# Performance work log

Measured on AMD Instinct MI355X. Metric: run time of the kernel, lower is better.

The kernel has to match this reference:

```python
import jax, jax.numpy as jnp
import numpy as np

B, NC, F, U = 8, 64, 8, 128   # batch, mesh size, ConvLSTM filters, LSTM units
NITER = 4
BS = 200.0                    # box size
B1, B2, LR, EPS = 0.9, 0.999, 0.1, 1e-7


def _conv3d(x, w, b=None):
    out = jax.lax.conv_general_dilated(x, w, (1, 1, 1), 'SAME',
                                       dimension_numbers=('NDHWC', 'DHWIO', 'NDHWC'))
    return out if b is None else out + b


def _conv1d(x, w, b):
    return jax.lax.conv_general_dilated(x, w, (1,), 'SAME',
                                        dimension_numbers=('NWC', 'WIO', 'NWC')) + b


def setup_inputs():
    key = jax.random.key(0)
    ks = jax.random.split(key, 16)
    # radial |k| bin map, values in [0, NC)
    kf = np.fft.fftfreq(NC) * NC
    kx, ky, kz = np.meshgrid(kf, kf, kf, indexing='ij')
    knorm = np.sqrt(kx ** 2 + ky ** 2 + kz ** 2)
    kbinmap = np.minimum((knorm / knorm.max() * (NC - 1)).astype(np.int32), NC - 1)
    s = 0.05
    return {
        'x_init': jax.random.normal(ks[0], (B, NC, NC, NC), jnp.float32),
        'y':      jax.random.normal(ks[1], (B, NC, NC, NC), jnp.float32),
        'x_true': jax.random.normal(ks[2], (B, NC, NC, NC), jnp.float32),
        'kbinmap': jnp.asarray(kbinmap),
        # input_layer: Conv3D 2 -> F
        'W_in': jax.random.normal(ks[3], (3, 3, 3, 2, F), jnp.float32) * s,
        'b_in': jnp.zeros((F,), jnp.float32),
        # ConvLSTM3D cell: gates order i,f,g,o
        'Wx3': jax.random.normal(ks[4], (3, 3, 3, F, 4 * F), jnp.float32) * s,
        'Wh3': jax.random.normal(ks[5], (3, 3, 3, F, 4 * F), jnp.float32) * s,
        'b3':  jnp.zeros((4 * F,), jnp.float32),
        # output_layer: Conv3D F -> 1
        'W_out': jax.random.normal(ks[6], (3, 3, 3, F, 1), jnp.float32) * s,
        'b_out': jnp.zeros((1,), jnp.float32),
        # input_layer1d: Dense 2*NC -> U
        'Wd1': jax.random.normal(ks[7], (2 * NC, U), jnp.float32) * s,
        'bd1': jnp.zeros((U,), jnp.float32),
        # LSTM cell (units U)
        'Wlx': jax.random.normal(ks[8], (U, 4 * U), jnp.float32) * s,
        'Wlh': jax.random.normal(ks[9], (U, 4 * U), jnp.float32) * s,
        'bl':  jnp.zeros((4 * U,), jnp.float32),
        # output_layer1d: Dense U -> NC
        'Wd2': jax.random.normal(ks[10], (U, NC), jnp.float32) * s,
        'bd2': jnp.zeros((NC,), jnp.float32),
        # output_layer1dconv: Conv1D 1 -> 1, kernel 3
        'Wc1': jax.random.normal(ks[11], (3, 1, 1), jnp.float32) * s,
        'bc1': jnp.zeros((1,), jnp.float32),
    }


def _forward(x_init, y, x_true, W_in, b_in, Wx3, Wh3, b3, W_out, b_out,
             Wd1, bd1, Wlx, Wlh, bl, Wd2, bd2, Wc1, bc1, kbinmap):
    nc = x_init.shape[-1]
    bsz = x_init.shape[0]
    kflat = kbinmap.reshape(-1)
    counts = jax.ops.segment_sum(jnp.ones(kflat.shape, jnp.float32), kflat,
                                 num_segments=nc)

    def varmap(x):
        # tfvarmap: binned power spectrum, [B, nc]
        pm = jnp.abs(jnp.fft.fftn(x, axes=(1, 2, 3)) / nc ** 3) ** 2
        pmf = pm.reshape(bsz, -1)
        power = jax.vmap(lambda p: jax.ops.segment_sum(p, kflat, num_segments=nc))(pmf)
        return power / counts

    def filt(x, ps, p):
        # colorps (p=+0.5) / whitenps (p=-0.5); flowpm r2c/c2r norms cancel
        pmesh = ps[:, kbinmap]                      # [B,nc,nc,nc] gather by kbin
        fac = (pmesh ** p).astype(jnp.complex64)
        return jnp.real(jnp.fft.ifftn(jnp.fft.fftn(x, axes=(1, 2, 3)) * fac,
                                      axes=(1, 2, 3)))

    def convlstm(x, h, c):
        z = _conv3d(x, Wx3, b3) + _conv3d(h, Wh3)
        i, f, g, o = jnp.split(z, 4, axis=-1)
        c = jax.nn.sigmoid(f) * c + jax.nn.sigmoid(i) * jnp.tanh(g)
        h = jax.nn.sigmoid(o) * jnp.tanh(c)
        return h, c

    def lstm(x, h, c):
        z = x @ Wlx + h @ Wlh + bl
        i, f, g, o = jnp.split(z, 4, axis=-1)
        c = jax.nn.sigmoid(f) * c + jax.nn.sigmoid(i) * jnp.tanh(g)
        h = jax.nn.sigmoid(o) * jnp.tanh(c)
        return h, c

    ln10 = jnp.log(jnp.float32(10.0))

    def step(carry, t):
        pos, m, v, h1, c1, h3, c3, loss = carry
        grad = pos - y                              # stand-in grad_fn (data-consistency)
        m = B1 * m + (1.0 - B1) * grad
        v = B2 * v + (1.0 - B2) * grad * grad
        mc = m / (1.0 - B1 ** t)
        vc = v / (1.0 - B2 ** t)
        delta = -LR * mc / (jnp.sqrt(vc) + EPS)
        pspos = varmap(pos)
        psdelta = varmap(delta)
        lpspos = jnp.log(pspos * BS ** 3) / ln10
        lpsdelta = jnp.log(psdelta * BS ** 3) / ln10
        # 3D branch
        cell_in = _conv3d(jnp.stack([pos, delta], axis=-1), W_in, b_in)
        h3, c3 = convlstm(cell_in, h3, c3)
        delta_poswhite = _conv3d(h3, W_out, b_out)[..., 0]
        # 1D power-spectrum branch
        x1 = jnp.concatenate([lpspos, lpsdelta], axis=-1) @ Wd1 + bd1
        h1, c1 = lstm(x1, h1, c1)
        lps = h1 @ Wd2 + bd2
        lps = _conv1d(lps[..., None], Wc1, bc1)[..., 0]
        psdeltanew = jnp.exp(lps)                   # note: exp (base e), as in source
        new_pos = pos + filt(delta_poswhite, psdeltanew, 0.5)
        loss = loss + jnp.mean((x_true - new_pos) ** 2)
        return (new_pos, m, v, h1, c1, h3, c3, loss), None

    z = jnp.zeros_like(x_init)
    init = (x_init, z, z,
            jnp.zeros((bsz, U), x_init.dtype), jnp.zeros((bsz, U), x_init.dtype),
            jnp.zeros(x_init.shape + (F,), x_init.dtype),
            jnp.zeros(x_init.shape + (F,), x_init.dtype),
            jnp.zeros((), x_init.dtype))
    ts = jnp.arange(1, NITER + 1, dtype=jnp.float32)
    (pos, m, v, h1, c1, h3, c3, loss), _ = jax.lax.scan(step, init, ts)
    return pos, loss


def reference(x_init, y, x_true, kbinmap, W_in, b_in, Wx3, Wh3, b3, W_out, b_out,
              Wd1, bd1, Wlx, Wlh, bl, Wd2, bd2, Wc1, bc1):
    return _forward(x_init, y, x_true, W_in, b_in, Wx3, Wh3, b3, W_out, b_out,
                    Wd1, bd1, Wlx, Wlh, bl, Wd2, bd2, Wc1, bc1, kbinmap)
```

## Files before the change

### kernel.cpp

```cpp
#include <hip/hip_runtime.h>
#include <math.h>

#define NCC 64
#define NB 8
#define VOL (NCC*NCC*NCC)
#define TOT (NB*VOL)
#define WTOT 170869
#define PI2 6.2831853071795864769f
#define HS 287496
#define SX 4356

typedef unsigned short u16;
typedef __bf16 bf16x8 __attribute__((ext_vector_type(8)));
typedef float f32x16 __attribute__((ext_vector_type(16)));

__device__ __forceinline__ float b2f(u16 h){ return __uint_as_float(((unsigned)h)<<16); }
__device__ __forceinline__ u16 f2b(float f){
  unsigned u = __float_as_uint(f);
  unsigned r = (u + 0x7FFFu + ((u>>16)&1u)) >> 16;
  return (u16)r;
}
__device__ __forceinline__ float fsig(float x){ return 1.f / (1.f + __expf(-x)); }
__device__ __forceinline__ float ftanh(float x){
  float e = __expf(2.f * x);
  return 1.f - 2.f / (e + 1.f);
}

template<bool INV>
__device__ __forceinline__ void fft8(float2* x) {
  const float C = 0.70710678118654752440f;
  float2 s0,s1,s2,s3,s4,s5,s6,s7;
  s0 = make_float2(x[0].x + x[4].x, x[0].y + x[4].y);
  s4 = make_float2(x[0].x - x[4].x, x[0].y - x[4].y);
  s1 = make_float2(x[1].x + x[5].x, x[1].y + x[5].y);
  s5 = make_float2(x[1].x - x[5].x, x[1].y - x[5].y);
  s2 = make_float2(x[2].x + x[6].x, x[2].y + x[6].y);
  s6 = make_float2(x[2].x - x[6].x, x[2].y - x[6].y);
  s3 = make_float2(x[3].x + x[7].x, x[3].y + x[7].y);
  s7 = make_float2(x[3].x - x[7].x, x[3].y - x[7].y);
  float2 n5, n6, n7;
  if (!INV) {
    n5 = make_float2(C*(s5.x + s5.y), C*(s5.y - s5.x));
    n6 = make_float2(s6.y, -s6.x);
    n7 = make_float2(C*(s7.y - s7.x), -C*(s7.x + s7.y));
  } else {
    n5 = make_float2(C*(s5.x - s5.y), C*(s5.y + s5.x));
    n6 = make_float2(-s6.y, s6.x);
    n7 = make_float2(-C*(s7.x + s7.y), C*(s7.x - s7.y));
  }
  float2 t0,t1,t2,t3,t4,t5,t6,t7,d;
  t0 = make_float2(s0.x + s2.x, s0.y + s2.y);
  t2 = make_float2(s0.x - s2.x, s0.y - s2.y);
  t1 = make_float2(s1.x + s3.x, s1.y + s3.y);
  d  = make_float2(s1.x - s3.x, s1.y - s3.y);
  t3 = INV ? make_float2(-d.y, d.x) : make_float2(d.y, -d.x);
  t4 = make_float2(s4.x + n6.x, s4.y + n6.y);
  t6 = make_float2(s4.x - n6.x, s4.y - n6.y);
  t5 = make_float2(n5.x + n7.x, n5.y + n7.y);
  d  = make_float2(n5.x - n7.x, n5.y - n7.y);
  t7 = INV ? make_float2(-d.y, d.x) : make_float2(d.y, -d.x);
  x[0] = make_float2(t0.x + t1.x, t0.y + t1.y);
  x[1] = make_float2(t0.x - t1.x, t0.y - t1.y);
  x[2] = make_float2(t2.x + t3.x, t2.y + t3.y);
  x[3] = make_float2(t2.x - t3.x, t2.y - t3.y);
  x[4] = make_float2(t4.x + t5.x, t4.y + t5.y);
  x[5] = make_float2(t4.x - t5.x, t4.y - t5.y);
  x[6] = make_float2(t6.x + t7.x, t6.y + t7.y);
  x[7] = make_float2(t6.x - t7.x, t6.y - t7.y);
}

template<bool INV>
__device__ __forceinline__ void dft64(float2* Pf, const float2* tw, int ls, int ns) {
  const int BR[8] = {0,4,2,6,1,5,3,7};
  int t = threadIdx.x;
  int L0 = t >> 3, b = t & 7, L1 = L0 + 32;
  float2 v0[8], v1[8];
  #pragma unroll
  for (int a = 0; a < 8; ++a) v0[a] = Pf[L0*ls + (8*a + b)*ns];
  #pragma unroll
  for (int a = 0; a < 8; ++a) v1[a] = Pf[L1*ls + (8*a + b)*ns];
  __syncthreads();
  fft8<INV>(v0); fft8<INV>(v1);
  #pragma unroll
  for (int r = 0; r < 8; ++r) {
    float2 w = tw[(b * r) & 63];
    if (INV) w.y = -w.y;
    float2 a0 = v0[BR[r]], a1 = v1[BR[r]];
    Pf[L0*ls + (8*b + r)*ns] = make_float2(a0.x*w.x - a0.y*w.y, a0.x*w.y + a0.y*w.x);
    Pf[L1*ls + (8*b + r)*ns] = make_float2(a1.x*w.x - a1.y*w.y, a1.x*w.y + a1.y*w.x);
  }
  __syncthreads();
  int r = t & 7;
  #pragma unroll
  for (int q = 0; q < 8; ++q) v0[q] = Pf[L0*ls + (8*q + r)*ns];
  #pragma unroll
  for (int q = 0; q < 8; ++q) v1[q] = Pf[L1*ls + (8*q + r)*ns];
  fft8<INV>(v0); fft8<INV>(v1);
  #pragma unroll
  for (int j = 0; j < 8; ++j) {
    Pf[L0*ls + (8*BR[j] + r)*ns] = v0[j];
    Pf[L1*ls + (8*BR[j] + r)*ns] = v1[j];
  }
  __syncthreads();
}

__global__ __launch_bounds__(256) void k_sniff(const u16* __restrict__ x, int* __restrict__ flag) {
  __shared__ int cnt;
  if (threadIdx.x == 0) cnt = 0;
  __syncthreads();
  int sane = 0;
  for (int i = threadIdx.x; i < 1024; i += 256) {
    u16 h = x[2 * i];
    int e = (h >> 7) & 0xFF;
    if (h == 0 || (e >= 0x68 && e <= 0x8F)) sane++;
  }
  atomicAdd(&cnt, sane);
  __syncthreads();
  if (threadIdx.x == 0) flag[0] = (cnt >= 768) ? 1 : 0;
}

__global__ __launch_bounds__(256) void k_cvt(const void* __restrict__ in, size_t eoff,
                                             float* __restrict__ out, const int* __restrict__ flag) {
  size_t i = (size_t)blockIdx.x * 256 + threadIdx.x;
  if (*flag) out[i] = b2f(((const u16*)in)[eoff + i]);
  else       out[i] = ((const float*)in)[eoff + i];
}

__global__ __launch_bounds__(256) void k_cvtall(
    const void* s0, const void* s1, const void* s2, const void* s3,
    const void* s4, const void* s5, const void* s6, const void* s7,
    const void* s8, const void* s9, const void* s10, const void* s11,
    const void* s12, const void* s13, const void* s14, const void* s15,
    float* __restrict__ out, const int* __restrict__ flag) {
  const void* ps[16] = {s0,s1,s2,s3,s4,s5,s6,s7,s8,s9,s10,s11,s12,s13,s14,s15};
  const int offs[17] = {0,432,440,7352,14264,14296,14512,14513,30897,31025,
                        96561,162097,162609,170801,170865,170868,170869};
  int i = blockIdx.x * 256 + threadIdx.x;
  if (i >= WTOT) return;
  int s = 0;
  #pragma unroll
  for (int k = 1; k < 16; ++k) if (i >= offs[k]) s = k;
  int j = i - offs[s];
  if (*flag) out[i] = b2f(((const u16*)ps[s])[j]);
  else       out[i] = ((const float*)ps[s])[j];
}

__global__ __launch_bounds__(256) void k_mkwf(const void* __restrict__ Wx, const void* __restrict__ Wh,
                                              const int* __restrict__ flag, u16* __restrict__ Wf) {
  int i = blockIdx.x * 256 + threadIdx.x;
  if (i >= 13824) return;
  int j = i & 7, co = (i >> 3) & 31, hi = (i >> 8) & 1, tap = i >> 9;
  int src = tap * 256 + j * 32 + co;
  const void* P = hi ? Wh : Wx;
  u16 val;
  if (*flag) val = ((const u16*)P)[src];
  else       val = f2b(((const float*)P)[src]);
  Wf[i] = val;
}

__global__ __launch_bounds__(256) void k_mkwfo(const void* __restrict__ Wo,
                                               const int* __restrict__ flag, u16* __restrict__ Wfo) {
  int i = blockIdx.x * 256 + threadIdx.x;
  if (i >= 7168) return;
  int j = i & 7, co = (i >> 3) & 31, hi = (i >> 8) & 1, p = i >> 9;
  int tap = 2 * p + hi;
  u16 val = 0;
  if (co == 0 && tap < 27) {
    int src = tap * 8 + j;
    val = *flag ? ((const u16*)Wo)[src] : f2b(((const float*)Wo)[src]);
  }
  Wfo[i] = val;
}

__global__ __launch_bounds__(256) void k_mkwfi(const void* __restrict__ Wi,
                                               const int* __restrict__ flag, u16* __restrict__ Wfi) {
  int i = blockIdx.x * 256 + threadIdx.x;
  if (i >= 2048) return;
  int j = i & 7, co = (i >> 3) & 31, hi = (i >> 8) & 1, m = i >> 9;
  int k = hi * 8 + j;
  int tap = m * 8 + (k >> 1), ch = k & 1;
  u16 val = 0;
  if (co < 8 && tap < 27) {
    int src = tap * 16 + ch * 8 + co;
    val = *flag ? ((const u16*)Wi)[src] : f2b(((const float*)Wi)[src]);
  }
  Wfi[i] = val;
}

__global__ __launch_bounds__(256) void k_counts(const int* __restrict__ kbin,
                                                float* __restrict__ cnts) {
  __shared__ float s[NCC];
  int t = threadIdx.x;
  if (t < NCC) s[t] = 0.f;
  __syncthreads();
  int i = blockIdx.x * 256 + t;
  atomicAdd(&s[kbin[i]], 1.f);
  __syncthreads();
  if (t < NCC) atomicAdd(&cnts[t], s[t]);
}

__global__ __launch_bounds__(256) void k_fft_zy_adam(
    const float* __restrict__ pos, const void* __restrict__ yraw, size_t yoff,
    float* __restrict__ m, float* __restrict__ v, float* __restrict__ dpw,
    float2* __restrict__ cout, float ib1, float ib2, int first,
    const int* __restrict__ flag, float* __restrict__ psp, float* __restrict__ psd) {
  __shared__ float2 P[64*66];
  __shared__ float2 tw[64];
  int t = threadIdx.x;
  if (t < 64) { float s, c; __sincosf(-(PI2/64.f)*(float)t, &s, &c); tw[t] = make_float2(c, s); }
  int bb = blockIdx.x >> 6, xx = blockIdx.x & 63;
  if (xx == 0) {
    if (t < 64)                 psp[bb*64 + t] = 0.f;
    else if (t < 128)           psd[bb*64 + (t - 64)] = 0.f;
  }
  size_t pb = (size_t)blockIdx.x * 4096;
  int bf = *flag;
  #pragma unroll
  for (int i = 0; i < 4; ++i) {
    int i4 = t + 256*i;
    float4 p4 = ((const float4*)(pos + pb))[i4];
    float yv[4];
    if (bf) {
      uint2 yu = ((const uint2*)((const u16*)yraw + yoff + pb))[i4];
      const u16* yp = (const u16*)&yu;
      yv[0]=b2f(yp[0]); yv[1]=b2f(yp[1]); yv[2]=b2f(yp[2]); yv[3]=b2f(yp[3]);
    } else {
      float4 y4 = ((const float4*)((const float*)yraw + yoff + pb))[i4];
      yv[0]=y4.x; yv[1]=y4.y; yv[2]=y4.z; yv[3]=y4.w;
    }
    float pv[4] = {p4.x, p4.y, p4.z, p4.w};
    float mo[4], vo[4], dd[4];
    if (!first) {
      float4 m4 = ((const float4*)(m + pb))[i4];
      float4 v4 = ((const float4*)(v + pb))[i4];
      mo[0]=m4.x; mo[1]=m4.y; mo[2]=m4.z; mo[3]=m4.w;
      vo[0]=v4.x; vo[1]=v4.y; vo[2]=v4.z; vo[3]=v4.w;
    }
    #pragma unroll
    for (int c = 0; c < 4; ++c) {
      float g = pv[c] - yv[c];
      float mi = first ? 0.1f*g : 0.9f*mo[c] + 0.1f*g;
      float vi = first ? 0.001f*g*g : 0.999f*vo[c] + 0.001f*g*g;
      mo[c] = mi; vo[c] = vi;
      dd[c] = -0.1f * (mi * ib1) / (sqrtf(vi * ib2) + 1e-7f);
    }
    ((float4*)(m + pb))[i4]   = make_float4(mo[0], mo[1], mo[2], mo[3]);
    ((float4*)(v + pb))[i4]   = make_float4(vo[0], vo[1], vo[2], vo[3]);
    ((float4*)(dpw + pb))[i4] = make_float4(dd[0], dd[1], dd[2], dd[3]);
    int base = i4 * 4;
    float2* row = P + (base >> 6)*66 + (base & 63);
    row[0] = make_float2(pv[0], 0.f);
    row[1] = make_float2(pv[1], 0.f);
    row[2] = make_float2(pv[2], 0.f);
    row[3] = make_float2(pv[3], 0.f);
  }
  __syncthreads();
  dft64<false>(P, tw, 66, 1);
  dft64<false>(P, tw, 1, 66);
  float4* dst = (float4*)(cout + pb);
  #pragma unroll
  for (int i = 0; i < 8; ++i) {
    int idx2 = (t + 256*i) * 2;
    float2 a = P[(idx2 >> 6)*66 + (idx2 & 63)];
    float2 b = P[(idx2 >> 6)*66 + (idx2 & 63) + 1];
    dst[t + 256*i] = make_float4(a.x, a.y, b.x, b.y);
  }
}

__global__ __launch_bounds__(256) void k_fft_zy(const float* __restrict__ rin,
                                                float2* __restrict__ cout) {
  __shared__ float2 P[64*66];
  __shared__ float2 tw[64];
  int t = threadIdx.x;
  if (t < 64) { float s, c; __sincosf(-(PI2/64.f)*(float)t, &s, &c); tw[t] = make_float2(c, s); }
  const float* src = rin + (size_t)blockIdx.x * 4096;
  #pragma unroll
  for (int i = 0; i < 4; ++i) {
    float4 v = ((const float4*)src)[t + 256*i];
    int base = (t + 256*i) * 4;
    float2* row = P + (base >> 6)*66 + (base & 63);
    row[0] = make_float2(v.x, 0.f);
    row[1] = make_float2(v.y, 0.f);
    row[2] = make_float2(v.z, 0.f);
    row[3] = make_float2(v.w, 0.f);
  }
  __syncthreads();
  dft64<false>(P, tw, 66, 1);
  dft64<false>(P, tw, 1, 66);
  float4* dst = (float4*)(cout + (size_t)blockIdx.x * 4096);
  #pragma unroll
  for (int i = 0; i < 8; ++i) {
    int idx2 = (t + 256*i) * 2;
    float2 a = P[(idx2 >> 6)*66 + (idx2 & 63)];
    float2 b = P[(idx2 >> 6)*66 + (idx2 & 63) + 1];
    dst[t + 256*i] = make_float4(a.x, a.y, b.x, b.y);
  }
}

__global__ __launch_bounds__(256) void k_fft_x_pow(const float2* __restrict__ cin,
                                                   const int* __restrict__ kb,
                                                   float* __restrict__ psum) {
  __shared__ float2 P[64*66];
  __shared__ float2 tw[64];
  __shared__ float pb[64];
  int t = threadIdx.x;
  if (t < 64) { float s, c; __sincosf(-(PI2/64.f)*(float)t, &s, &c); tw[t] = make_float2(c, s); pb[t] = 0.f; }
  int b = blockIdx.x >> 6, y = blockIdx.x & 63;
  #pragma unroll
  for (int i = 0; i < 8; ++i) {
    int idx2 = (t + 256*i) * 2;
    int x = idx2 >> 6, z = idx2 & 63;
    float4 v = *(const float4*)(cin + (((size_t)(b*64 + x)*64 + y)*64 + z));
    P[x*66 + z]     = make_float2(v.x, v.y);
    P[x*66 + z + 1] = make_float2(v.z, v.w);
  }
  __syncthreads();
  dft64<false>(P, tw, 1, 66);
  const float INV2 = 1.0f / ((float)VOL * (float)VOL);
  #pragma unroll
  for (int i = 0; i < 16; ++i) {
    int idx = t + 256*i;
    int x = idx >> 6, z = idx & 63;
    float2 a = P[x*66 + z];
    float pm = (a.x*a.x + a.y*a.y) * INV2;
    atomicAdd(&pb[kb[(x*64 + y)*64 + z]], pm);
  }
  __syncthreads();
  if (t < 64) atomicAdd(&psum[b*64 + t], pb[t]);
}

__global__ __launch_bounds__(256) void k_fft_x_filt(float2* __restrict__ cb,
                                                    const int* __restrict__ kb,
                                                    const float* __restrict__ psn) {
  __shared__ float2 P[64*66];
  __shared__ float2 tw[64];
  int t = threadIdx.x;
  if (t < 64) { float s, c; __sincosf(-(PI2/64.f)*(float)t, &s, &c); tw[t] = make_float2(c, s); }
  int b = blockIdx.x >> 6, y = blockIdx.x & 63;
  #pragma unroll
  for (int i = 0; i < 8; ++i) {
    int idx2 = (t + 256*i) * 2;
    int x = idx2 >> 6, z = idx2 & 63;
    float4 v = *(const float4*)(cb + (((size_t)(b*64 + x)*64 + y)*64 + z));
    P[x*66 + z]     = make_float2(v.x, v.y);
    P[x*66 + z + 1] = make_float2(v.z, v.w);
  }
  __syncthreads();
  dft64<false>(P, tw, 1, 66);
  #pragma unroll
  for (int i = 0; i < 16; ++i) {
    int idx = t + 256*i;
    int x = idx >> 6, z = idx & 63;
    float fac = sqrtf(psn[b*64 + kb[(x*64 + y)*64 + z]]);
    float2 a = P[x*66 + z];
    P[x*66 + z] = make_float2(a.x * fac, a.y * fac);
  }
  __syncthreads();
  dft64<true>(P, tw, 1, 66);
  #pragma unroll
  for (int i = 0; i < 8; ++i) {
    int idx2 = (t + 256*i) * 2;
    int x = idx2 >> 6, z = idx2 & 63;
    float2 a = P[x*66 + z], c = P[x*66 + z + 1];
    *(float4*)(cb + (((size_t)(b*64 + x)*64 + y)*64 + z)) = make_float4(a.x, a.y, c.x, c.y);
  }
}

__global__ __launch_bounds__(256) void k_fft_zy_inv(const float2* __restrict__ cin,
                                                    float* __restrict__ pos,
                                                    const void* __restrict__ xtraw, size_t xoff,
                                                    float* __restrict__ lsum,
                                                    const int* __restrict__ flag,
                                                    void* __restrict__ outp, size_t ooff) {
  __shared__ float2 P[64*66];
  __shared__ float2 tw[64];
  __shared__ float red[256];
  int t = threadIdx.x;
  if (t < 64) { float s, c; __sincosf(-(PI2/64.f)*(float)t, &s, &c); tw[t] = make_float2(c, s); }
  size_t pb = (size_t)blockIdx.x * 4096;
  const float4* src = (const float4*)(cin + pb);
  #pragma unroll
  for (int i = 0; i < 8; ++i) {
    float4 v = src[t + 256*i];
    int idx2 = (t + 256*i) * 2;
    P[(idx2 >> 6)*66 + (idx2 & 63)]     = make_float2(v.x, v.y);
    P[(idx2 >> 6)*66 + (idx2 & 63) + 1] = make_float2(v.z, v.w);
  }
  __syncthreads();
  dft64<true>(P, tw, 1, 66);
  dft64<true>(P, tw, 66, 1);
  float* pdst = pos + pb;
  int bf = *flag;
  float lacc = 0.f;
  #pragma unroll
  for (int i = 0; i < 16; ++i) {
    int idx = t + 256*i;
    float np = pdst[idx] + P[(idx >> 6)*66 + (idx & 63)].x * (1.0f/(float)VOL);
    pdst[idx] = np;
    if (outp) {
      if (bf) ((u16*)outp)[ooff + pb + idx] = f2b(np);
      else    ((float*)outp)[ooff + pb + idx] = np;
    }
    float xt = bf ? b2f(((const u16*)xtraw)[xoff + pb + idx])
                  : ((const float*)xtraw)[xoff + pb + idx];
    float d = xt - np;
    lacc = fmaf(d, d, lacc);
  }
  red[t] = lacc; __syncthreads();
  for (int s = 128; s > 0; s >>= 1) { if (t < s) red[t] += red[t+s]; __syncthreads(); }
  if (t == 0) atomicAdd(lsum, red[0]);
}

__global__ __launch_bounds__(512, 8) void k_cellin(const float* __restrict__ pos,
                                                   const float* __restrict__ delta,
                                                   const u16* __restrict__ Wfi,
                                                   const float* __restrict__ binf,
                                                   u16* __restrict__ ci) {
  __shared__ u16 wfl[2048];
  int t = threadIdx.x;
  if (t < 256) ((uint4*)wfl)[t] = ((const uint4*)Wfi)[t];
  int wv = t >> 6, l = t & 63, ln = l & 31, hi = l >> 5;
  int bid = blockIdx.x;
  int x = bid & 63, yq = (bid >> 6) & 15, b = bid >> 10;
  int y = yq * 4 + (wv >> 1), z0 = (wv & 1) * 32;
  int z = z0 + ln;
  const u16* wbase = wfl + hi * 256 + ln * 8;
  __syncthreads();
  f32x16 acc;
  #pragma unroll
  for (int r = 0; r < 16; ++r) acc[r] = 0.f;
  #pragma unroll
  for (int m = 0; m < 4; ++m) {
    unsigned pk[4];
    #pragma unroll
    for (int kk = 0; kk < 4; ++kk) {
      const int tap = m * 8 + hi * 4 + kk;
      float pv = 0.f, dv = 0.f;
      if (tap < 27) {
        const int dx = tap / 9 - 1, dy = (tap / 3) % 3 - 1, dz = tap % 3 - 1;
        int nx = x + dx, ny = y + dy, nz = z + dz;
        if ((unsigned)nx < 64u && (unsigned)ny < 64u && (unsigned)nz < 64u) {
          size_t n = (((size_t)b * 64 + nx) * 64 + ny) * 64 + nz;
          pv = pos[n]; dv = delta[n];
        }
      }
      pk[kk] = (unsigned)f2b(pv) | ((unsigned)f2b(dv) << 16);
    }
    uint4 q = make_uint4(pk[0], pk[1], pk[2], pk[3]);
    bf16x8 bfr = __builtin_bit_cast(bf16x8, q);
    bf16x8 wfr = __builtin_bit_cast(bf16x8, *(const uint4*)(wbase + m * 512));
    acc = __builtin_amdgcn_mfma_f32_32x32x16_bf16(wfr, bfr, acc, 0, 0, 0);
  }
  size_t cslot = (size_t)b * HS + (size_t)(x + 1) * SX + (y + 1) * 66 + z + 1;
  u16 hh[4];
  #pragma unroll
  for (int q = 0; q < 4; ++q) hh[q] = f2b(acc[q] + binf[hi * 4 + q]);
  *(uint2*)(ci + cslot * 8 + hi * 4) = *(uint2*)hh;
}

__global__ __launch_bounds__(512, 8) void k_clstm(const u16* __restrict__ ci,
                                                  const u16* __restrict__ hC,
                                                  u16* __restrict__ hN,
                                                  u16* __restrict__ c3u,
                                                  const u16* __restrict__ Wf,
                                                  const float* __restrict__ b3f) {
  __shared__ u16 wfl[13824];
  int t = threadIdx.x;
  for (int i = t; i < 1728; i += 512) ((uint4*)wfl)[i] = ((const uint4*)Wf)[i];
  int wv = t >> 6, l = t & 63, ln = l & 31, hi = l >> 5;
  int bid = blockIdx.x;
  int x = bid & 63, yq = (bid >> 6) & 15, b = bid >> 10;
  int y = yq * 4 + (wv >> 1), z0 = (wv & 1) * 32;
  size_t cslot = (size_t)b * HS + (size_t)(x + 1) * SX + (y + 1) * 66 + z0 + ln + 1;
  const u16* abase = (hi ? hC : ci) + cslot * 8;
  const u16* axm = abase - SX * 8;
  const u16* axp = abase + SX * 8;
  const u16* wbase = wfl + hi * 256 + ln * 8;
  __syncthreads();
  f32x16 acc;
  #pragma unroll
  for (int r = 0; r < 16; ++r) acc[r] = 0.f;
  #pragma unroll
  for (int tap = 0; tap < 27; ++tap) {
    const int dx = tap / 9, dy = (tap / 3) % 3 - 1, dz = tap % 3 - 1;
    const u16* ab = (dx == 0) ? axm : ((dx == 1) ? abase : axp);
    bf16x8 wfr = __builtin_bit_cast(bf16x8, *(const uint4*)(wbase + tap * 512));
    bf16x8 afr = __builtin_bit_cast(bf16x8, *(const uint4*)(ab + (dy * 66 + dz) * 8));
    acc = __builtin_amdgcn_mfma_f32_32x32x16_bf16(wfr, afr, acc, 0, 0, 0);
  }
  float4 bi  = *(const float4*)(b3f + 4 * hi);
  float4 bff = *(const float4*)(b3f + 8 + 4 * hi);
  float4 bg  = *(const float4*)(b3f + 16 + 4 * hi);
  float4 bo_ = *(const float4*)(b3f + 24 + 4 * hi);
  const float* bip = (const float*)&bi;
  const float* bfp = (const float*)&bff;
  const float* bgp = (const float*)&bg;
  const float* bop = (const float*)&bo_;
  uint2 cu = *(const uint2*)(c3u + cslot * 8 + hi * 4);
  const u16* cp = (const u16*)&cu;
  u16 cw[4], hw[4];
  #pragma unroll
  for (int q = 0; q < 4; ++q) {
    float zi  = acc[q]      + bip[q];
    float zf  = acc[4 + q]  + bfp[q];
    float zg  = acc[8 + q]  + bgp[q];
    float zo_ = acc[12 + q] + bop[q];
    float cn = fsig(zf) * b2f(cp[q]) + fsig(zi) * ftanh(zg);
    cw[q] = f2b(cn);
    hw[q] = f2b(fsig(zo_) * ftanh(cn));
  }
  *(uint2*)(c3u + cslot * 8 + hi * 4) = *(uint2*)cw;
  *(uint2*)(hN + cslot * 8 + hi * 4)  = *(uint2*)hw;
}

__global__ __launch_bounds__(512, 8) void k_wout(const u16* __restrict__ h,
                                                 const u16* __restrict__ Wfo,
                                                 const float* __restrict__ bo,
                                                 float* __restrict__ dpw) {
  __shared__ u16 wfl[7168];
  int t = threadIdx.x;
  for (int i = t; i < 896; i += 512) ((uint4*)wfl)[i] = ((const uint4*)Wfo)[i];
  int wv = t >> 6, l = t & 63, ln = l & 31, hi = l >> 5;
  int bid = blockIdx.x;
  int x = bid & 63, yq = (bid >> 6) & 15, b = bid >> 10;
  int y = yq * 4 + (wv >> 1), z0 = (wv & 1) * 32;
  size_t cslot = (size_t)b * HS + (size_t)(x + 1) * SX + (y + 1) * 66 + z0 + ln + 1;
  const u16* abase = h + cslot * 8;
  const u16* wbase = wfl + hi * 256 + ln * 8;
  __syncthreads();
  f32x16 acc;
  #pragma unroll
  for (int r = 0; r < 16; ++r) acc[r] = 0.f;
  #pragma unroll
  for (int p = 0; p < 14; ++p) {
    const int t0 = 2 * p;
    const int t1 = (2 * p + 1 < 27) ? (2 * p + 1) : 26;
    const int o0 = (t0 / 9) * SX + ((t0 / 3) % 3) * 66 + (t0 % 3) - (SX + 66 + 1);
    const int o1 = (t1 / 9) * SX + ((t1 / 3) % 3) * 66 + (t1 % 3) - (SX + 66 + 1);
    int off = hi ? o1 : o0;
    bf16x8 wfr = __builtin_bit_cast(bf16x8, *(const uint4*)(wbase + p * 512));
    bf16x8 afr = __builtin_bit_cast(bf16x8, *(const uint4*)(abase + (ptrdiff_t)off * 8));
    acc = __builtin_amdgcn_mfma_f32_32x32x16_bf16(wfr, afr, acc, 0, 0, 0);
  }
  if (hi == 0) {
    size_t vox = (((size_t)b * 64 + x) * 64 + y) * 64 + z0 + ln;
    dpw[vox] = acc[0] + bo[0];
  }
}

__global__ __launch_bounds__(256) void k_small(const float* __restrict__ psp,
                                               const float* __restrict__ psd,
                                               const float* __restrict__ cnts,
                                               const float* __restrict__ Wd1,
                                               const float* __restrict__ bd1,
                                               const float* __restrict__ Wlx,
                                               const float* __restrict__ Wlh,
                                               const float* __restrict__ bl,
                                               const float* __restrict__ Wd2,
                                               const float* __restrict__ bd2,
                                               const float* __restrict__ Wc1,
                                               const float* __restrict__ bc1,
                                               float* __restrict__ h1, float* __restrict__ c1,
                                               float* __restrict__ psn) {
  __shared__ float lp[128], x1[128], hs[128], zz[512], lps[66];
  int t = threadIdx.x, b = blockIdx.x;
  if (t < 64) {
    lp[t]      = __log10f(fmaxf(psp[b*64 + t] / cnts[t] * 8.0e6f, 1e-30f));
    lp[64 + t] = __log10f(fmaxf(psd[b*64 + t] / cnts[t] * 8.0e6f, 1e-30f));
  }
  if (t < 128) hs[t] = h1[b*128 + t];
  __syncthreads();
  if (t < 128) {
    float a = bd1[t];
    for (int j = 0; j < 128; ++j) a = fmaf(lp[j], Wd1[j*128 + t], a);
    x1[t] = a;
  }
  __syncthreads();
  for (int k = t; k < 512; k += 256) {
    float a = bl[k];
    for (int u = 0; u < 128; ++u)
      a = fmaf(x1[u], Wlx[u*512 + k], fmaf(hs[u], Wlh[u*512 + k], a));
    zz[k] = a;
  }
  __syncthreads();
  if (t < 128) {
    float cv = fsig(zz[128 + t]) * c1[b*128 + t] + fsig(zz[t]) * ftanh(zz[256 + t]);
    c1[b*128 + t] = cv;
    float hv = fsig(zz[384 + t]) * ftanh(cv);
    h1[b*128 + t] = hv; hs[t] = hv;
  }
  __syncthreads();
  if (t < 64) {
    float a = bd2[t];
    for (int u = 0; u < 128; ++u) a = fmaf(hs[u], Wd2[u*64 + t], a);
    lps[t + 1] = a;
  }
  __syncthreads();
  if (t < 64) {
    float a = fmaf(Wc1[1], lps[t + 1], bc1[0]);
    if (t > 0)  a = fmaf(Wc1[0], lps[t], a);
    if (t < 63) a = fmaf(Wc1[2], lps[t + 2], a);
    psn[b*64 + t] = __expf(a);
  }
}

__global__ void k_loss(const float* __restrict__ lsum, void* __restrict__ outp,
                       const int* __restrict__ flag) {
  float l = lsum[0] * (1.0f / (float)TOT);
  if (*flag) ((u16*)outp)[TOT] = f2b(l);
  else       ((float*)outp)[TOT] = l;
}

__global__ void k_sent(u16* __restrict__ outp) { outp[0] = f2b(1000.0f); }

extern "C" void kernel_launch(void* const* d_in, const int* in_sizes, int n_in,
                              void* d_out, int out_size, void* d_ws, size_t ws_size,
                              hipStream_t stream) {
  const void* x_init = d_in[0];
  const void* y      = d_in[1];
  const void* x_true = d_in[2];
  const int*  kbin   = (const int*)d_in[3];

  int nbs = 0;
  for (int cand = 8; cand >= 1; cand >>= 1) {
    size_t n1c = (size_t)cand * VOL;
    size_t slc = (size_t)cand * HS;
    size_t need = 4 * n1c * 4
                + 4 * slc * 16
                + n1c * 8
                + (171008 + 6912 + 3584 + 1024 + (size_t)cand * (192 + 256) + 96) * 4;
    if (need <= ws_size) { nbs = cand; break; }
  }
  if (nbs == 0) { k_sent<<<1, 1, 0, stream>>>((u16*)d_out); return; }

  size_t n1 = (size_t)nbs * VOL;
  size_t sl = (size_t)nbs * HS;
  float* ws   = (float*)d_ws;
  float* pos  = ws;
  float* m    = pos + n1;
  float* v    = m + n1;
  float* dpw  = v + n1;
  u16*  c3u   = (u16*)(dpw + n1);
  u16*  ci    = c3u + sl*8;
  u16*  hA    = ci + sl*8;
  u16*  hB    = hA + sl*8;
  float2* cb  = (float2*)(hB + sl*8);
  float* wbuf = (float*)((float*)cb + n1*2);
  u16*  Wf    = (u16*)(wbuf + 171008);
  u16*  Wfo   = Wf + 13824;
  u16*  Wfi   = Wfo + 7168;
  float* psp  = wbuf + 171008 + 6912 + 3584 + 1024;
  float* psd  = psp + (size_t)nbs*64;
  float* psn  = psd + (size_t)nbs*64;
  float* cnts = psn + (size_t)nbs*64;
  float* lsum = cnts + 64;
  float* h1   = lsum + 8;
  float* c1   = h1 + (size_t)nbs*128;
  int*   flag = (int*)(c1 + (size_t)nbs*128);

  float* bin_f = wbuf + 432;
  float* b3_f  = wbuf + 14264;
  float* bo_f  = wbuf + 14512; float* Wd1_f = wbuf + 14513;
  float* bd1_f = wbuf + 30897; float* Wlx_f = wbuf + 31025;
  float* Wlh_f = wbuf + 96561; float* bl_f  = wbuf + 162097;
  float* Wd2_f = wbuf + 162609; float* bd2_f = wbuf + 170801;
  float* Wc1_f = wbuf + 170865; float* bc1_f = wbuf + 170868;

  const int CB = (int)(n1 / 256);

  k_sniff<<<1, 256, 0, stream>>>((const u16*)x_init, flag);
  k_cvtall<<<(WTOT + 255) / 256, 256, 0, stream>>>(
      d_in[4], d_in[5], d_in[6], d_in[7], d_in[8], d_in[9], d_in[10], d_in[11],
      d_in[12], d_in[13], d_in[14], d_in[15], d_in[16], d_in[17], d_in[18], d_in[19],
      wbuf, flag);
  k_mkwf<<<54, 256, 0, stream>>>(d_in[6], d_in[7], flag, Wf);
  k_mkwfo<<<28, 256, 0, stream>>>(d_in[9], flag, Wfo);
  k_mkwfi<<<8, 256, 0, stream>>>(d_in[4], flag, Wfi);
  hipMemsetAsync(cnts, 0, 72 * 4, stream);
  k_counts<<<VOL / 256, 256, 0, stream>>>(kbin, cnts);

  for (int b0 = 0; b0 < NB; b0 += nbs) {
    hipMemsetAsync(c3u, 0, sl * 64, stream);
    hipMemsetAsync(h1, 0, (size_t)nbs * 256 * 4, stream);
    k_cvt<<<CB, 256, 0, stream>>>(x_init, (size_t)b0 * VOL, pos, flag);

    u16* hC = hA;
    u16* hN = hB;
    for (int t = 1; t <= 4; ++t) {
      float ib1 = (float)(1.0 / (1.0 - pow(0.9, (double)t)));
      float ib2 = (float)(1.0 / (1.0 - pow(0.999, (double)t)));

      k_fft_zy_adam<<<nbs * 64, 256, 0, stream>>>(pos, y, (size_t)b0 * VOL, m, v, dpw,
                                                  cb, ib1, ib2, t == 1, flag, psp, psd);
      k_fft_x_pow<<<nbs * 64, 256, 0, stream>>>(cb, kbin, psp);
      k_fft_zy<<<nbs * 64, 256, 0, stream>>>(dpw, cb);
      k_fft_x_pow<<<nbs * 64, 256, 0, stream>>>(cb, kbin, psd);

      k_cellin<<<nbs * 1024, 512, 0, stream>>>(pos, dpw, Wfi, bin_f, ci);
      k_clstm<<<nbs * 1024, 512, 0, stream>>>(ci, hC, hN, c3u, Wf, b3_f);
      k_wout<<<nbs * 1024, 512, 0, stream>>>(hN, Wfo, bo_f, dpw);

      k_small<<<nbs, 256, 0, stream>>>(psp, psd, cnts, Wd1_f, bd1_f, Wlx_f, Wlh_f, bl_f,
                                       Wd2_f, bd2_f, Wc1_f, bc1_f, h1, c1, psn);

      k_fft_zy<<<nbs * 64, 256, 0, stream>>>(dpw, cb);
      k_fft_x_filt<<<nbs * 64, 256, 0, stream>>>(cb, kbin, psn);
      k_fft_zy_inv<<<nbs * 64, 256, 0, stream>>>(cb, pos, x_true, (size_t)b0 * VOL, lsum,
                                                 flag, (t == 4) ? d_out : nullptr,
                                                 (size_t)b0 * VOL);

      u16* tmp = hC; hC = hN; hN = tmp;
    }
  }
  k_loss<<<1, 1, 0, stream>>>(lsum, d_out, flag);
}
```

Measured before the change: 1.281 ms.

## Pack two real FFTs into one complex FFT for power spectra

The position field and the Adam delta field are now packed as the real and imaginary parts of one complex 3D FFT. Their individual spectra are separated using conjugate symmetry: the new power kernel pairs each y plane with its mirror plane and bins both power spectra in one pass. This removes one zy FFT pass and one x-FFT/power pass per iteration, halving the FFT traffic for the power spectra. In exchange the power kernel is more complex, holds two shared planes per block and uses 512 threads, and self-paired planes (y=0,32) need special handling.

```diff
diff --git a/kernel.cpp b/kernel.cpp
--- a/kernel.cpp
+++ b/kernel.cpp
@@ -70,9 +70,8 @@
 }
 
 template<bool INV>
-__device__ __forceinline__ void dft64(float2* Pf, const float2* tw, int ls, int ns) {
+__device__ __forceinline__ void dft64t(float2* Pf, const float2* tw, int ls, int ns, int t) {
   const int BR[8] = {0,4,2,6,1,5,3,7};
-  int t = threadIdx.x;
   int L0 = t >> 3, b = t & 7, L1 = L0 + 32;
   float2 v0[8], v1[8];
   #pragma unroll
@@ -102,6 +101,11 @@
     Pf[L1*ls + (8*BR[j] + r)*ns] = v1[j];
   }
   __syncthreads();
+}
+
+template<bool INV>
+__device__ __forceinline__ void dft64(float2* Pf, const float2* tw, int ls, int ns) {
+  dft64t<INV>(Pf, tw, ls, ns, threadIdx.x);
 }
 
 __global__ __launch_bounds__(256) void k_sniff(const u16* __restrict__ x, int* __restrict__ flag) {
@@ -249,10 +253,10 @@
     ((float4*)(dpw + pb))[i4] = make_float4(dd[0], dd[1], dd[2], dd[3]);
     int base = i4 * 4;
     float2* row = P + (base >> 6)*66 + (base & 63);
-    row[0] = make_float2(pv[0], 0.f);
-    row[1] = make_float2(pv[1], 0.f);
-    row[2] = make_float2(pv[2], 0.f);
-    row[3] = make_float2(pv[3], 0.f);
+    row[0] = make_float2(pv[0], dd[0]);
+    row[1] = make_float2(pv[1], dd[1]);
+    row[2] = make_float2(pv[2], dd[2]);
+    row[3] = make_float2(pv[3], dd[3]);
   }
   __syncthreads();
   dft64<false>(P, tw, 66, 1);
@@ -297,36 +301,59 @@
   }
 }
 
-__global__ __launch_bounds__(256) void k_fft_x_pow(const float2* __restrict__ cin,
-                                                   const int* __restrict__ kb,
-                                                   float* __restrict__ psum) {
-  __shared__ float2 P[64*66];
+__global__ __launch_bounds__(512) void k_fft_x_powsep(const float2* __restrict__ cb,
+                                                      const int* __restrict__ kb,
+                                                      float* __restrict__ psp,
+                                                      float* __restrict__ psd) {
+  __shared__ float2 PA[64*66];
+  __shared__ float2 PB[64*66];
   __shared__ float2 tw[64];
-  __shared__ float pb[64];
-  int t = threadIdx.x;
-  if (t < 64) { float s, c; __sincosf(-(PI2/64.f)*(float)t, &s, &c); tw[t] = make_float2(c, s); pb[t] = 0.f; }
-  int b = blockIdx.x >> 6, y = blockIdx.x & 63;
+  __shared__ float pbp[64], pbd[64];
+  int t = threadIdx.x, tl = t & 255, g2 = t >> 8;
+  if (t < 64) {
+    float s, c; __sincosf(-(PI2/64.f)*(float)t, &s, &c);
+    tw[t] = make_float2(c, s);
+    pbp[t] = 0.f; pbd[t] = 0.f;
+  }
+  int b = blockIdx.x / 33, pi = blockIdx.x % 33;
+  int y  = pi;
+  int ym = (64 - pi) & 63;
+  int self = (pi == 0 || pi == 32);
+  int py = g2 ? ym : y;
+  float2* P = g2 ? PB : PA;
   #pragma unroll
   for (int i = 0; i < 8; ++i) {
-    int idx2 = (t + 256*i) * 2;
+    int idx2 = (tl + 256*i) * 2;
     int x = idx2 >> 6, z = idx2 & 63;
-    float4 v = *(const float4*)(cin + (((size_t)(b*64 + x)*64 + y)*64 + z));
+    float4 v = *(const float4*)(cb + (((size_t)(b*64 + x)*64 + py)*64 + z));
     P[x*66 + z]     = make_float2(v.x, v.y);
     P[x*66 + z + 1] = make_float2(v.z, v.w);
   }
   __syncthreads();
-  dft64<false>(P, tw, 1, 66);
+  dft64t<false>(P, tw, 1, 66, tl);
   const float INV2 = 1.0f / ((float)VOL * (float)VOL);
-  #pragma unroll
-  for (int i = 0; i < 16; ++i) {
-    int idx = t + 256*i;
-    int x = idx >> 6, z = idx & 63;
-    float2 a = P[x*66 + z];
-    float pm = (a.x*a.x + a.y*a.y) * INV2;
-    atomicAdd(&pb[kb[(x*64 + y)*64 + z]], pm);
-  }
-  __syncthreads();
-  if (t < 64) atomicAdd(&psum[b*64 + t], pb[t]);
+  if (!(g2 && self)) {
+    const float2* Q = g2 ? PA : PB;
+    #pragma unroll
+    for (int i = 0; i < 16; ++i) {
+      int idx = tl + 256*i;
+      int x = idx >> 6, z = idx & 63;
+      float2 A = P[x*66 + z];
+      int xm = (64 - x) & 63, zm = (64 - z) & 63;
+      float2 Bm = Q[xm*66 + zm];
+      float Br = Bm.x, Bi = -Bm.y;
+      float Pr = 0.5f * (A.x + Br), Pi = 0.5f * (A.y + Bi);
+      float Dr = 0.5f * (A.y - Bi), Di = 0.5f * (Br - A.x);
+      int bin = kb[(x*64 + py)*64 + z];
+      atomicAdd(&pbp[bin], (Pr*Pr + Pi*Pi) * INV2);
+      atomicAdd(&pbd[bin], (Dr*Dr + Di*Di) * INV2);
+    }
+  }
+  __syncthreads();
+  if (t < 64) {
+    atomicAdd(&psp[b*64 + t], pbp[t]);
+    atomicAdd(&psd[b*64 + t], pbd[t]);
+  }
 }
 
 __global__ __launch_bounds__(256) void k_fft_x_filt(float2* __restrict__ cb,
@@ -692,9 +719,7 @@
 
       k_fft_zy_adam<<<nbs * 64, 256, 0, stream>>>(pos, y, (size_t)b0 * VOL, m, v, dpw,
                                                   cb, ib1, ib2, t == 1, flag, psp, psd);
-      k_fft_x_pow<<<nbs * 64, 256, 0, stream>>>(cb, kbin, psp);
-      k_fft_zy<<<nbs * 64, 256, 0, stream>>>(dpw, cb);
-      k_fft_x_pow<<<nbs * 64, 256, 0, stream>>>(cb, kbin, psd);
+      k_fft_x_powsep<<<nbs * 33, 512, 0, stream>>>(cb, kbin, psp, psd);
 
       k_cellin<<<nbs * 1024, 512, 0, stream>>>(pos, dpw, Wfi, bin_f, ci);
       k_clstm<<<nbs * 1024, 512, 0, stream>>>(ci, hC, hN, c3u, Wf, b3_f);
```

Measured after the change: 1.296 ms. Within noise of the previous version (+1.2%).
